# Kernel optimization log

Hardware: AMD Instinct MI355X
Metric: run time of the kernel (lower is better)

The kernel has to match this reference:

```python
import jax, jax.numpy as jnp
import numpy as np

N_BINS = 15


def setup_inputs() -> dict:
    key = jax.random.key(0)
    k1, k2 = jax.random.split(key)
    N, C = 500000, 100
    logits = jax.random.normal(k1, (N, C), dtype=jnp.float32)
    labels = jax.random.randint(k2, (N,), 0, C, dtype=jnp.int64)
    return {"logits": logits, "labels": labels}


def _classwise_ece(logits, labels, n_bins=N_BINS):
    # Fused equivalent of the per-class, per-bin double loop.
    # Bins are (lower, upper] with boundaries linspace(0,1,n_bins+1),
    # so bin index = ceil(p * n_bins) - 1; p == 0 falls in NO bin.
    probs = jax.nn.softmax(logits, axis=1)            # [N, C]
    N, C = probs.shape
    valid = probs > 0.0                               # p==0 matched by no (lower, upper] bin
    bin_idx = jnp.clip(jnp.ceil(probs * n_bins).astype(jnp.int32) - 1, 0, n_bins - 1)

    class_ids = jnp.arange(C, dtype=jnp.int32)[None, :]          # [1, C]
    key = (jnp.broadcast_to(class_ids * n_bins, probs.shape) + bin_idx).reshape(-1)  # [N*C]

    w = valid.astype(probs.dtype)
    correct = (labels[:, None] == class_ids).astype(probs.dtype)  # labels_in_class

    num_seg = C * n_bins
    count = jax.ops.segment_sum(w.reshape(-1), key, num_segments=num_seg).reshape(C, n_bins)
    conf_sum = jax.ops.segment_sum((probs * w).reshape(-1), key, num_segments=num_seg).reshape(C, n_bins)
    acc_sum = jax.ops.segment_sum((correct * w).reshape(-1), key, num_segments=num_seg).reshape(C, n_bins)

    # |avg_conf - acc| * prop_in_bin == |conf_sum - acc_sum| / N; empty bins give 0.
    per_class_sce = jnp.sum(jnp.abs(conf_sum - acc_sum), axis=1) / N   # [C]
    sce = jnp.mean(per_class_sce)
    return sce, per_class_sce


def reference(logits, labels):
    return _classwise_ece(logits, labels)
```

## Files before the change

### kernel.cpp

```cpp
#include <hip/hip_runtime.h>
#include <math.h>

#define NCLS 100
#define NBINS 15
#define NSEG (NCLS * NBINS)
#define NTOT (2 * NSEG + NCLS)
#define PSTRIDE 3104
#define RPI 8
#define GMAIN 1024

__device__ __forceinline__ void fadd(float* p, float v) { unsafeAtomicAdd(p, v); }

__device__ __forceinline__ float readlane_f(float x, int l) {
    return __builtin_bit_cast(float, __builtin_amdgcn_readlane(__builtin_bit_cast(int, x), l));
}

template <int CTRL>
__device__ __forceinline__ float dpp_add(float x) {
    int y = __builtin_amdgcn_update_dpp(0, __builtin_bit_cast(int, x),
                                        CTRL, 0xf, 0xf, true);
    return x + __builtin_bit_cast(float, y);
}

__device__ __forceinline__ void load_tile(
    const float* __restrict__ logits, const int* __restrict__ labels,
    int base, int N, int lane, bool act,
    float (&e0)[RPI], float (&e1)[RPI], int& labv)
{
    labv = labels[min(base + lane, N - 1)];
    const float* rp = logits + (size_t)base * NCLS + 2 * lane;
    if (base + RPI <= N) {
        #pragma unroll
        for (int r = 0; r < RPI; ++r) {
            float2 v = make_float2(-1000.f, -1000.f);
            if (act) v = *(const float2*)(rp + (size_t)r * NCLS);
            e0[r] = v.x; e1[r] = v.y;
        }
    } else {
        #pragma unroll
        for (int r = 0; r < RPI; ++r) {
            float2 v = make_float2(-1000.f, -1000.f);
            if (act && (base + r) < N) v = *(const float2*)(rp + (size_t)r * NCLS);
            e0[r] = v.x; e1[r] = v.y;
        }
    }
}

__device__ __forceinline__ void compute_tile(
    int base, int N, int lane, bool act, int c0, int c1,
    float (&e0)[RPI], float (&e1)[RPI], int labv,
    float& t0, float& t1, float* s_conf, float* s_acc)
{
    float s[RPI];
    #pragma unroll
    for (int r = 0; r < RPI; ++r) {
        e0[r] = __expf(e0[r]);
        e1[r] = __expf(e1[r]);
        s[r] = e0[r] + e1[r];
    }
    #pragma unroll
    for (int r = 0; r < RPI; ++r) s[r] = dpp_add<0x111>(s[r]);
    #pragma unroll
    for (int r = 0; r < RPI; ++r) s[r] = dpp_add<0x112>(s[r]);
    #pragma unroll
    for (int r = 0; r < RPI; ++r) s[r] = dpp_add<0x114>(s[r]);
    #pragma unroll
    for (int r = 0; r < RPI; ++r) s[r] = dpp_add<0x118>(s[r]);
    #pragma unroll
    for (int r = 0; r < RPI; ++r) s[r] = dpp_add<0x142>(s[r]);
    #pragma unroll
    for (int r = 0; r < RPI; ++r) s[r] = dpp_add<0x143>(s[r]);

    #pragma unroll
    for (int r = 0; r < RPI; ++r) {
        const float tot = readlane_f(s[r], 63);
        const float inv = __builtin_amdgcn_rcpf(fmaxf(tot, 1e-30f));
        const int lab = (base + r < N)
                      ? __builtin_amdgcn_readlane(labv, r) : -1;
        const float p0 = e0[r] * inv;
        const float p1 = e1[r] * inv;
        t0 += p0;
        t1 += p1;
        if (act) {
            int b0 = min((int)ceilf(p0 * 15.f) - 1, NBINS - 1);
            if (b0 >= 1) fadd(&s_conf[c0 * NBINS + b0], p0);
            if (c0 == lab) fadd(&s_acc[c0 * NBINS + max(b0, 0)], 1.f);
            int b1 = min((int)ceilf(p1 * 15.f) - 1, NBINS - 1);
            if (b1 >= 1) fadd(&s_conf[c1 * NBINS + b1], p1);
            if (c1 == lab) fadd(&s_acc[c1 * NBINS + max(b1, 0)], 1.f);
        }
    }
}

__global__ __launch_bounds__(256, 4) void ece_main_kernel(
    const float* __restrict__ logits,
    const int* __restrict__ labels,
    float* __restrict__ g_hist,
    float* __restrict__ parts,
    int N)
{
    __shared__ float s_conf[NSEG];
    __shared__ float s_acc[NSEG];
    __shared__ float s_total[NCLS];
    for (int i = threadIdx.x; i < NSEG; i += 256) { s_conf[i] = 0.f; s_acc[i] = 0.f; }
    if (threadIdx.x < NCLS) s_total[threadIdx.x] = 0.f;
    __syncthreads();

    const int lane   = threadIdx.x & 63;
    const int wave   = threadIdx.x >> 6;
    const int gwave  = blockIdx.x * 4 + wave;
    const int nwaves = gridDim.x * 4;
    const bool act   = (lane < NCLS / 2);
    const int c0 = 2 * lane;
    const int c1 = 2 * lane + 1;

    float t0 = 0.f, t1 = 0.f;

    float A0[RPI], A1[RPI], B0[RPI], B1[RPI];
    int labA = 0, labB = 0;
    const int step = nwaves * RPI;
    int base = gwave * RPI;
    bool curA = true;
    if (base < N) load_tile(logits, labels, base, N, lane, act, A0, A1, labA);
    while (base < N) {
        const int nxt = base + step;
        if (curA) {
            if (nxt < N) {
                load_tile(logits, labels, nxt, N, lane, act, B0, B1, labB);
                __builtin_amdgcn_sched_barrier(0);
            }
            compute_tile(base, N, lane, act, c0, c1, A0, A1, labA, t0, t1, s_conf, s_acc);
        } else {
            if (nxt < N) {
                load_tile(logits, labels, nxt, N, lane, act, A0, A1, labA);
                __builtin_amdgcn_sched_barrier(0);
            }
            compute_tile(base, N, lane, act, c0, c1, B0, B1, labB, t0, t1, s_conf, s_acc);
        }
        curA = !curA;
        base = nxt;
    }

    if (act) { fadd(&s_total[c0], t0); fadd(&s_total[c1], t1); }
    __syncthreads();

    if (parts) {
        float* my = parts + (size_t)blockIdx.x * PSTRIDE;
        for (int i = threadIdx.x; i < NSEG; i += 256) {
            __builtin_nontemporal_store(s_conf[i], &my[i]);
            __builtin_nontemporal_store(s_acc[i], &my[NSEG + i]);
        }
        if (threadIdx.x < NCLS)
            __builtin_nontemporal_store(s_total[threadIdx.x], &my[2 * NSEG + threadIdx.x]);
    } else {
        for (int i = threadIdx.x; i < NSEG; i += 256) {
            float v = s_conf[i]; if (v != 0.f) fadd(&g_hist[i], v);
            float a = s_acc[i];  if (a != 0.f) fadd(&g_hist[NSEG + i], a);
        }
        if (threadIdx.x < NCLS) {
            float t = s_total[threadIdx.x];
            if (t != 0.f) fadd(&g_hist[2 * NSEG + threadIdx.x], t);
        }
    }
}

__global__ __launch_bounds__(256) void ece_reduce_kernel(
    const float* __restrict__ parts, float* __restrict__ g_hist, int nparts)
{
    const int lane = threadIdx.x & 63;
    const int wave = threadIdx.x >> 6;
    const int cell = blockIdx.x * 64 + lane;
    const int nchunks = gridDim.y * 4;
    const int chunk = blockIdx.y * 4 + wave;
    const int per = nparts / nchunks;
    float s = 0.f;
    if (cell < NTOT) {
        const float* bp = parts + (size_t)chunk * per * PSTRIDE + cell;
        #pragma unroll 8
        for (int p = 0; p < per; ++p)
            s += __builtin_nontemporal_load(&bp[(size_t)p * PSTRIDE]);
    }
    __shared__ float red[4][64];
    red[wave][lane] = s;
    __syncthreads();
    if (wave == 0) {
        float v = red[0][lane] + red[1][lane] + red[2][lane] + red[3][lane];
        if (cell < NTOT && v != 0.f) fadd(&g_hist[cell], v);
    }
}

__global__ __launch_bounds__(128) void ece_final_kernel(
    const float* __restrict__ g_hist,
    float* __restrict__ out,
    float invN)
{
    __shared__ float red[128];
    const int t = threadIdx.x;
    float s = 0.f;
    if (t < NCLS) {
        float conf0 = g_hist[2 * NSEG + t];
        float sum = 0.f;
        #pragma unroll
        for (int b = 1; b < NBINS; ++b) {
            float cb = g_hist[t * NBINS + b];
            float ab = g_hist[NSEG + t * NBINS + b];
            conf0 -= cb;
            sum += fabsf(cb - ab);
        }
        sum += fabsf(conf0 - g_hist[NSEG + t * NBINS + 0]);
        s = sum * invN;
        out[1 + t] = s;
    }
    red[t] = s;
    __syncthreads();
    #pragma unroll
    for (int off = 64; off > 0; off >>= 1) {
        if (t < off) red[t] += red[t + off];
        __syncthreads();
    }
    if (t == 0) out[0] = red[0] * (1.0f / (float)NCLS);
}

extern "C" void kernel_launch(void* const* d_in, const int* in_sizes, int n_in,
                              void* d_out, int out_size, void* d_ws, size_t ws_size,
                              hipStream_t stream)
{
    const float* logits = (const float*)d_in[0];
    const int*   labels = (const int*)d_in[1];
    const int N = in_sizes[1];
    float* out = (float*)d_out;

    float* g_hist = (float*)d_ws;
    const size_t parts_off = ((size_t)NTOT * sizeof(float) + 255) & ~(size_t)255;
    const size_t need = parts_off + (size_t)GMAIN * PSTRIDE * sizeof(float);
    float* parts = (ws_size >= need) ? (float*)((char*)d_ws + parts_off) : nullptr;

    (void)hipMemsetAsync(d_ws, 0, (size_t)NTOT * sizeof(float), stream);

    ece_main_kernel<<<GMAIN, 256, 0, stream>>>(logits, labels, g_hist, parts, N);
    if (parts) {
        dim3 g2((NTOT + 63) / 64, 4);
        ece_reduce_kernel<<<g2, 256, 0, stream>>>(parts, g_hist, GMAIN);
    }
    ece_final_kernel<<<1, 128, 0, stream>>>(g_hist, out, 1.0f / (float)N);
}
```

Before: 299.9 us.

## Process two rows per wave with float4 loads and simplify partial reduction

```diff
diff --git a/kernel.cpp b/kernel.cpp
--- a/kernel.cpp
+++ b/kernel.cpp
@@ -6,7 +6,8 @@
 #define NSEG (NCLS * NBINS)
 #define NTOT (2 * NSEG + NCLS)
 #define PSTRIDE 3104
-#define RPI 8
+#define RPI 16
+#define SLOTS (RPI / 2)
 #define GMAIN 1024
 
 __device__ __forceinline__ void fadd(float* p, float v) { unsafeAtomicAdd(p, v); }
@@ -24,70 +25,82 @@
 
 __device__ __forceinline__ void load_tile(
     const float* __restrict__ logits, const int* __restrict__ labels,
-    int base, int N, int lane, bool act,
-    float (&e0)[RPI], float (&e1)[RPI], int& labv)
+    int base, int N, int lane, int q, int h, bool act,
+    float4 (&e)[SLOTS], int& labv)
 {
     labv = labels[min(base + lane, N - 1)];
-    const float* rp = logits + (size_t)base * NCLS + 2 * lane;
+    const float* rp = logits + (size_t)(base + h) * NCLS + 4 * q;
     if (base + RPI <= N) {
         #pragma unroll
-        for (int r = 0; r < RPI; ++r) {
-            float2 v = make_float2(-1000.f, -1000.f);
-            if (act) v = *(const float2*)(rp + (size_t)r * NCLS);
-            e0[r] = v.x; e1[r] = v.y;
+        for (int k = 0; k < SLOTS; ++k) {
+            float4 v = make_float4(-1000.f, -1000.f, -1000.f, -1000.f);
+            if (act) v = *(const float4*)(rp + (size_t)(2 * k) * NCLS);
+            e[k] = v;
         }
     } else {
         #pragma unroll
-        for (int r = 0; r < RPI; ++r) {
-            float2 v = make_float2(-1000.f, -1000.f);
-            if (act && (base + r) < N) v = *(const float2*)(rp + (size_t)r * NCLS);
-            e0[r] = v.x; e1[r] = v.y;
+        for (int k = 0; k < SLOTS; ++k) {
+            float4 v = make_float4(-1000.f, -1000.f, -1000.f, -1000.f);
+            if (act && (base + 2 * k + h) < N)
+                v = *(const float4*)(rp + (size_t)(2 * k) * NCLS);
+            e[k] = v;
         }
     }
 }
 
 __device__ __forceinline__ void compute_tile(
-    int base, int N, int lane, bool act, int c0, int c1,
-    float (&e0)[RPI], float (&e1)[RPI], int labv,
-    float& t0, float& t1, float* s_conf, float* s_acc)
-{
-    float s[RPI];
-    #pragma unroll
-    for (int r = 0; r < RPI; ++r) {
-        e0[r] = __expf(e0[r]);
-        e1[r] = __expf(e1[r]);
-        s[r] = e0[r] + e1[r];
-    }
-    #pragma unroll
-    for (int r = 0; r < RPI; ++r) s[r] = dpp_add<0x111>(s[r]);
-    #pragma unroll
-    for (int r = 0; r < RPI; ++r) s[r] = dpp_add<0x112>(s[r]);
-    #pragma unroll
-    for (int r = 0; r < RPI; ++r) s[r] = dpp_add<0x114>(s[r]);
-    #pragma unroll
-    for (int r = 0; r < RPI; ++r) s[r] = dpp_add<0x118>(s[r]);
-    #pragma unroll
-    for (int r = 0; r < RPI; ++r) s[r] = dpp_add<0x142>(s[r]);
-    #pragma unroll
-    for (int r = 0; r < RPI; ++r) s[r] = dpp_add<0x143>(s[r]);
-
-    #pragma unroll
-    for (int r = 0; r < RPI; ++r) {
-        const float tot = readlane_f(s[r], 63);
-        const float inv = __builtin_amdgcn_rcpf(fmaxf(tot, 1e-30f));
-        const int lab = (base + r < N)
-                      ? __builtin_amdgcn_readlane(labv, r) : -1;
-        const float p0 = e0[r] * inv;
-        const float p1 = e1[r] * inv;
-        t0 += p0;
-        t1 += p1;
+    int base, int N, int q, int h, bool act,
+    float4 (&e)[SLOTS], int labv,
+    float (&t)[4], float* s_conf, float* s_acc)
+{
+    float s[SLOTS];
+    #pragma unroll
+    for (int k = 0; k < SLOTS; ++k) {
+        e[k].x = __expf(e[k].x); e[k].y = __expf(e[k].y);
+        e[k].z = __expf(e[k].z); e[k].w = __expf(e[k].w);
+        s[k] = (e[k].x + e[k].y) + (e[k].z + e[k].w);
+    }
+    #pragma unroll
+    for (int k = 0; k < SLOTS; ++k) s[k] = dpp_add<0x111>(s[k]);
+    #pragma unroll
+    for (int k = 0; k < SLOTS; ++k) s[k] = dpp_add<0x112>(s[k]);
+    #pragma unroll
+    for (int k = 0; k < SLOTS; ++k) s[k] = dpp_add<0x114>(s[k]);
+    #pragma unroll
+    for (int k = 0; k < SLOTS; ++k) s[k] = dpp_add<0x118>(s[k]);
+    #pragma unroll
+    for (int k = 0; k < SLOTS; ++k) s[k] = dpp_add<0x142>(s[k]);
+
+    #pragma unroll
+    for (int k = 0; k < SLOTS; ++k) {
+        const float inv_e = __builtin_amdgcn_rcpf(fmaxf(readlane_f(s[k], 31), 1e-30f));
+        const float inv_o = __builtin_amdgcn_rcpf(fmaxf(readlane_f(s[k], 63), 1e-30f));
+        const float inv = h ? inv_o : inv_e;
+        const int re = base + 2 * k;
+        const int lab_e = (re < N)     ? __builtin_amdgcn_readlane(labv, 2 * k)     : -1;
+        const int lab_o = (re + 1 < N) ? __builtin_amdgcn_readlane(labv, 2 * k + 1) : -1;
+        const int lab = h ? lab_o : lab_e;
+
+        const float p0 = e[k].x * inv;
+        const float p1 = e[k].y * inv;
+        const float p2 = e[k].z * inv;
+        const float p3 = e[k].w * inv;
+        t[0] += p0; t[1] += p1; t[2] += p2; t[3] += p3;
+
         if (act) {
+            const int c0 = 4 * q;
             int b0 = min((int)ceilf(p0 * 15.f) - 1, NBINS - 1);
-            if (b0 >= 1) fadd(&s_conf[c0 * NBINS + b0], p0);
-            if (c0 == lab) fadd(&s_acc[c0 * NBINS + max(b0, 0)], 1.f);
+            if (b0 >= 1) fadd(&s_conf[(c0 + 0) * NBINS + b0], p0);
+            if (c0 + 0 == lab) fadd(&s_acc[(c0 + 0) * NBINS + max(b0, 0)], 1.f);
             int b1 = min((int)ceilf(p1 * 15.f) - 1, NBINS - 1);
-            if (b1 >= 1) fadd(&s_conf[c1 * NBINS + b1], p1);
-            if (c1 == lab) fadd(&s_acc[c1 * NBINS + max(b1, 0)], 1.f);
+            if (b1 >= 1) fadd(&s_conf[(c0 + 1) * NBINS + b1], p1);
+            if (c0 + 1 == lab) fadd(&s_acc[(c0 + 1) * NBINS + max(b1, 0)], 1.f);
+            int b2 = min((int)ceilf(p2 * 15.f) - 1, NBINS - 1);
+            if (b2 >= 1) fadd(&s_conf[(c0 + 2) * NBINS + b2], p2);
+            if (c0 + 2 == lab) fadd(&s_acc[(c0 + 2) * NBINS + max(b2, 0)], 1.f);
+            int b3 = min((int)ceilf(p3 * 15.f) - 1, NBINS - 1);
+            if (b3 >= 1) fadd(&s_conf[(c0 + 3) * NBINS + b3], p3);
+            if (c0 + 3 == lab) fadd(&s_acc[(c0 + 3) * NBINS + max(b3, 0)], 1.f);
         }
     }
 }
@@ -110,38 +123,41 @@
     const int wave   = threadIdx.x >> 6;
     const int gwave  = blockIdx.x * 4 + wave;
     const int nwaves = gridDim.x * 4;
-    const bool act   = (lane < NCLS / 2);
-    const int c0 = 2 * lane;
-    const int c1 = 2 * lane + 1;
-
-    float t0 = 0.f, t1 = 0.f;
-
-    float A0[RPI], A1[RPI], B0[RPI], B1[RPI];
+    const int q      = lane & 31;
+    const int h      = lane >> 5;
+    const bool act   = (q < NCLS / 4);
+
+    float t[4] = {0.f, 0.f, 0.f, 0.f};
+
+    float4 A[SLOTS], B[SLOTS];
     int labA = 0, labB = 0;
     const int step = nwaves * RPI;
     int base = gwave * RPI;
     bool curA = true;
-    if (base < N) load_tile(logits, labels, base, N, lane, act, A0, A1, labA);
+    if (base < N) load_tile(logits, labels, base, N, lane, q, h, act, A, labA);
     while (base < N) {
         const int nxt = base + step;
         if (curA) {
             if (nxt < N) {
-                load_tile(logits, labels, nxt, N, lane, act, B0, B1, labB);
+                load_tile(logits, labels, nxt, N, lane, q, h, act, B, labB);
                 __builtin_amdgcn_sched_barrier(0);
             }
-            compute_tile(base, N, lane, act, c0, c1, A0, A1, labA, t0, t1, s_conf, s_acc);
+            compute_tile(base, N, q, h, act, A, labA, t, s_conf, s_acc);
         } else {
             if (nxt < N) {
-                load_tile(logits, labels, nxt, N, lane, act, A0, A1, labA);
+                load_tile(logits, labels, nxt, N, lane, q, h, act, A, labA);
                 __builtin_amdgcn_sched_barrier(0);
             }
-            compute_tile(base, N, lane, act, c0, c1, B0, B1, labB, t0, t1, s_conf, s_acc);
+            compute_tile(base, N, q, h, act, B, labB, t, s_conf, s_acc);
         }
         curA = !curA;
         base = nxt;
     }
 
-    if (act) { fadd(&s_total[c0], t0); fadd(&s_total[c1], t1); }
+    if (act) {
+        #pragma unroll
+        for (int j = 0; j < 4; ++j) fadd(&s_total[4 * q + j], t[j]);
+    }
     __syncthreads();
 
     if (parts) {
@@ -158,34 +174,34 @@
             float a = s_acc[i];  if (a != 0.f) fadd(&g_hist[NSEG + i], a);
         }
         if (threadIdx.x < NCLS) {
-            float t = s_total[threadIdx.x];
-            if (t != 0.f) fadd(&g_hist[2 * NSEG + threadIdx.x], t);
-        }
-    }
-}
-
-__global__ __launch_bounds__(256) void ece_reduce_kernel(
+            float tt = s_total[threadIdx.x];
+            if (tt != 0.f) fadd(&g_hist[2 * NSEG + threadIdx.x], tt);
+        }
+    }
+}
+
+__global__ __launch_bounds__(512) void ece_reduce_kernel(
     const float* __restrict__ parts, float* __restrict__ g_hist, int nparts)
 {
     const int lane = threadIdx.x & 63;
     const int wave = threadIdx.x >> 6;
     const int cell = blockIdx.x * 64 + lane;
-    const int nchunks = gridDim.y * 4;
-    const int chunk = blockIdx.y * 4 + wave;
-    const int per = nparts / nchunks;
+    const int per = nparts / 8;
     float s = 0.f;
     if (cell < NTOT) {
-        const float* bp = parts + (size_t)chunk * per * PSTRIDE + cell;
+        const float* bp = parts + (size_t)wave * per * PSTRIDE + cell;
         #pragma unroll 8
         for (int p = 0; p < per; ++p)
             s += __builtin_nontemporal_load(&bp[(size_t)p * PSTRIDE]);
     }
-    __shared__ float red[4][64];
+    __shared__ float red[8][64];
     red[wave][lane] = s;
     __syncthreads();
     if (wave == 0) {
-        float v = red[0][lane] + red[1][lane] + red[2][lane] + red[3][lane];
-        if (cell < NTOT && v != 0.f) fadd(&g_hist[cell], v);
+        float v = 0.f;
+        #pragma unroll
+        for (int w = 0; w < 8; ++w) v += red[w][lane];
+        if (cell < NTOT) g_hist[cell] = v;
     }
 }
 
@@ -235,12 +251,11 @@
     const size_t need = parts_off + (size_t)GMAIN * PSTRIDE * sizeof(float);
     float* parts = (ws_size >= need) ? (float*)((char*)d_ws + parts_off) : nullptr;
 
-    (void)hipMemsetAsync(d_ws, 0, (size_t)NTOT * sizeof(float), stream);
+    if (!parts)
+        (void)hipMemsetAsync(d_ws, 0, (size_t)NTOT * sizeof(float), stream);
 
     ece_main_kernel<<<GMAIN, 256, 0, stream>>>(logits, labels, g_hist, parts, N);
-    if (parts) {
-        dim3 g2((NTOT + 63) / 64, 4);
-        ece_reduce_kernel<<<g2, 256, 0, stream>>>(parts, g_hist, GMAIN);
-    }
+    if (parts)
+        ece_reduce_kernel<<<(NTOT + 63) / 64, 512, 0, stream>>>(parts, g_hist, GMAIN);
     ece_final_kernel<<<1, 128, 0, stream>>>(g_hist, out, 1.0f / (float)N);
 }
```

Measured after the change: 529.2 us. +76.4%, slower.
